# Kernel tuning notes

Measured on AMD Instinct MI355X. Metric: run time of the kernel, lower is better.

The kernel has to match this reference:

```python
import jax, jax.numpy as jnp
import numpy as np

N = 50000          # num nodes
E = 800000         # num edges (avg degree 16)
F_IN = 512         # num_feature
HID = 128          # hid
COM_LAMBDA = 1.0


def setup_inputs() -> dict:
    key = jax.random.key(0)
    k1, k2, k3, k4, k5, k6 = jax.random.split(key, 6)
    v_ori_vals = jax.random.uniform(k1, (E,), dtype=jnp.float32)
    feat = jax.random.normal(k2, (N, F_IN), dtype=jnp.float32)
    v_indices = jax.random.randint(k3, (2, E), 0, N, dtype=jnp.int64)
    # GraphConvolution params
    gcn_w = jax.random.normal(k4, (F_IN, HID), dtype=jnp.float32) / np.sqrt(F_IN)
    gcn_b = jnp.zeros((HID,), dtype=jnp.float32)
    # gen_mlp: Linear(2*hid, 1), xavier_normal init
    std = 1.414 * np.sqrt(2.0 / (2 * HID + 1))
    mlp_w = jax.random.normal(k5, (1, 2 * HID), dtype=jnp.float32) * std
    mlp_b = jnp.zeros((1,), dtype=jnp.float32)
    return {"v_ori_vals": v_ori_vals, "feat": feat, "v_indices": v_indices,
            "num_node": N, "gcn_w": gcn_w, "gcn_b": gcn_b,
            "mlp_w": mlp_w, "mlp_b": mlp_b}


def reference(v_ori_vals, feat, v_indices, num_node, gcn_w, gcn_b, mlp_w, mlp_b):
    row, col = v_indices[0], v_indices[1]
    # gen_gcn: emb = A @ (feat @ W) + b  (SpMM via segment_sum over edges)
    support = feat @ gcn_w                                      # [N, HID]
    emb = jax.ops.segment_sum(v_ori_vals[:, None] * support[col], row,
                              num_segments=num_node) + gcn_b    # [N, HID]
    # gather endpoints, concat, edge-scoring MLP (dropout = identity in eval)
    ff = jnp.concatenate([emb[row], emb[col]], axis=-1)         # [E, 2*HID]
    temp = (ff @ mlp_w.T + mlp_b).reshape(-1)                   # [E]
    # sparse row-wise softmax over columns (dim=1) -> segment softmax by row
    m = jax.ops.segment_max(temp, row, num_segments=num_node)   # [N]
    e = jnp.exp(temp - m[row])                                  # [E]
    s = jax.ops.segment_sum(e, row, num_segments=num_node)      # [N]
    pi = e / s[row]                                             # [E]
    # gen_v = v_ori + com_lambda * pi (values on the shared edge pattern)
    return v_ori_vals + COM_LAMBDA * pi
```

## Files before the change

kernel.cpp:

```cpp
#include <hip/hip_runtime.h>


typedef unsigned int u32;

#define RPB     128
#define CAP     3072
#define NB_MAX  512
#define SB      256

__global__ void k_prep(const float* __restrict__ W, const float* __restrict__ mw,
                       float* __restrict__ u2, u32* __restrict__ cnt,
                       int F, int H, int nb) {
  if (blockIdx.x == 0)
    for (int s = threadIdx.x; s < nb; s += blockDim.x) cnt[s] = 0;
  int f = blockIdx.x * blockDim.x + threadIdx.x;
  if (f >= F) return;
  const float4* wr = (const float4*)(W + (size_t)f * H);
  const float4* mv = (const float4*)(mw + H);
  float s = 0.f;
  for (int i = 0; i < H / 4; ++i) {
    float4 a = wr[i], b = mv[i];
    s = fmaf(a.x, b.x, fmaf(a.y, b.y, fmaf(a.z, b.z, fmaf(a.w, b.w, s))));
  }
  u2[f] = s;
}

template <int F>
__global__ void k_gemv(const float* __restrict__ feat, const float* __restrict__ u2,
                       float* __restrict__ q, int N) {
  const int lane = threadIdx.x & 63;
  const float4 ua = *(const float4*)(u2 + lane * 8);
  const float4 ub = *(const float4*)(u2 + lane * 8 + 4);
  const int wid = (blockIdx.x * blockDim.x + threadIdx.x) >> 6;
  const int nw  = (gridDim.x * blockDim.x) >> 6;
  for (int r = wid; r < N; r += nw) {
    const float* fr = feat + (size_t)r * F + lane * 8;
    float4 a = *(const float4*)fr;
    float4 b = *(const float4*)(fr + 4);
    float s = fmaf(a.x, ua.x, fmaf(a.y, ua.y, fmaf(a.z, ua.z,
              fmaf(a.w, ua.w, fmaf(b.x, ub.x, fmaf(b.y, ub.y,
              fmaf(b.z, ub.z, b.w * ub.w)))))));
    s += __shfl_xor(s, 32);
    s += __shfl_xor(s, 16);
    s += __shfl_xor(s, 8);
    s += __shfl_xor(s, 4);
    s += __shfl_xor(s, 2);
    s += __shfl_xor(s, 1);
    if (lane == 0) q[r] = s;
  }
}

__global__ void __launch_bounds__(1024)
k_sortscatter(const int* __restrict__ row, const int* __restrict__ col,
              const float* __restrict__ v, int E, int chunk,
              u32* __restrict__ cnt, uint2* __restrict__ rec8, int nb) {
  __shared__ u32 h[NB_MAX];
  __shared__ u32 start[NB_MAX];
  const int tid = threadIdx.x;
  for (int s = tid; s < nb; s += blockDim.x) h[s] = 0;
  __syncthreads();
  const int lo = blockIdx.x * chunk;
  const int hi = min(E, lo + chunk);
  for (int e = lo + tid; e < hi; e += blockDim.x)
    atomicAdd(&h[row[e] >> 7], 1u);
  __syncthreads();
  for (int s = tid; s < nb; s += blockDim.x) {
    u32 c = h[s];
    start[s] = c ? atomicAdd(&cnt[s], c) : 0u;
    h[s] = 0u;
  }
  __syncthreads();
  for (int e = lo + tid; e < hi; e += blockDim.x) {
    int r = row[e];
    int b = r >> 7;
    u32 rank = atomicAdd(&h[b], 1u);
    u32 off  = min(start[b] + rank, (u32)CAP - 1);
    rec8[(size_t)b * CAP + off] =
        make_uint2(((u32)col[e] << 7) | (u32)(r & 127),
                   __float_as_uint(v[e]));
  }
}

__global__ void __launch_bounds__(1024)
k_sum_t(const uint2* __restrict__ rec8, const u32* __restrict__ cnt,
        const float* __restrict__ q, float* __restrict__ t) {
  __shared__ float acc[RPB];
  const int b = blockIdx.x;
  const int tid = threadIdx.x;
  if (tid < RPB) acc[tid] = 0.f;
  __syncthreads();
  const u32 lo = (u32)b * CAP;
  const u32 n  = min(cnt[b], (u32)CAP);
  for (u32 i = tid; i < n; i += blockDim.x) {
    uint2 rr = rec8[lo + i];
    atomicAdd(&acc[rr.x & 127], q[rr.x >> 7] * __uint_as_float(rr.y));
  }
  __syncthreads();
  if (tid < RPB) t[b * RPB + tid] = __expf(acc[tid]);
}

__global__ void __launch_bounds__(1024)
k_sum_invS(const uint2* __restrict__ rec8, const u32* __restrict__ cnt,
           const float* __restrict__ t, float* __restrict__ invS) {
  __shared__ float acc[RPB];
  const int b = blockIdx.x;
  const int tid = threadIdx.x;
  if (tid < RPB) acc[tid] = 0.f;
  __syncthreads();
  const u32 lo = (u32)b * CAP;
  const u32 n  = min(cnt[b], (u32)CAP);
  for (u32 i = tid; i < n; i += blockDim.x) {
    uint2 rr = rec8[lo + i];
    atomicAdd(&acc[rr.x & 127], t[rr.x >> 7]);
  }
  __syncthreads();
  if (tid < RPB) invS[b * RPB + tid] = 1.0f / acc[tid];
}

__global__ void k_out(const int* __restrict__ row, const int* __restrict__ col,
                      const float* __restrict__ vori, const float* __restrict__ t,
                      const float* __restrict__ invS, float* __restrict__ out,
                      int E) {
  int e = blockIdx.x * blockDim.x + threadIdx.x;
  if (e >= E) return;
  out[e] = vori[e] + t[col[e]] * invS[row[e]];
}

__global__ void k_scatter_B_at(const int* __restrict__ row, const int* __restrict__ col,
                               const float* __restrict__ v, const float* __restrict__ q,
                               float* __restrict__ B, int E) {
  int e = blockIdx.x * blockDim.x + threadIdx.x;
  if (e >= E) return;
  atomicAdd(&B[row[e]], v[e] * q[col[e]]);
}
__global__ void k_node_t(const float* __restrict__ B, float* __restrict__ t, int N) {
  int n = blockIdx.x * blockDim.x + threadIdx.x;
  if (n < N) t[n] = __expf(B[n]);
}
__global__ void k_scatter_S_at(const int* __restrict__ row, const int* __restrict__ col,
                               const float* __restrict__ t, float* __restrict__ S, int E) {
  int e = blockIdx.x * blockDim.x + threadIdx.x;
  if (e >= E) return;
  atomicAdd(&S[row[e]], t[col[e]]);
}
__global__ void k_out_div(const int* __restrict__ row, const int* __restrict__ col,
                          const float* __restrict__ vori, const float* __restrict__ t,
                          const float* __restrict__ S, float* __restrict__ out, int E) {
  int e = blockIdx.x * blockDim.x + threadIdx.x;
  if (e >= E) return;
  out[e] = vori[e] + t[col[e]] / S[row[e]];
}

extern "C" void kernel_launch(void* const* d_in, const int* in_sizes, int n_in,
                              void* d_out, int out_size, void* d_ws, size_t ws_size,
                              hipStream_t stream) {
  const float* vori = (const float*)d_in[0];
  const float* feat = (const float*)d_in[1];
  const int*   vind = (const int*)d_in[2];
  const float* W    = (const float*)d_in[4];
  const float* mw   = (const float*)d_in[6];

  const int E = in_sizes[0];
  const int H = in_sizes[6] / 2;
  const int F = in_sizes[4] / H;
  const int N = in_sizes[1] / F;

  const int* row = vind;
  const int* col = vind + E;

  const int nb   = (N + RPB - 1) / RPB;
  const int npad = nb * RPB;

  float* ws   = (float*)d_ws;
  float* u2   = ws;
  float* q    = u2 + F;
  float* t    = q + N;
  float* invS = t + npad;
  u32*   cnt  = (u32*)(invS + npad);
  size_t hdr  = (size_t)((char*)(cnt + nb) - (char*)d_ws);
  hdr = (hdr + 15) & ~(size_t)15;
  uint2* rec8 = (uint2*)((char*)d_ws + hdr);
  size_t need = hdr + (size_t)nb * CAP * sizeof(uint2);

  const int eb = (E + 255) / 256;

  k_prep<<<(F + 255) / 256, 256, 0, stream>>>(W, mw, u2, cnt, F, H, nb);
  k_gemv<512><<<3125, 256, 0, stream>>>(feat, u2, q, N);

  if (ws_size >= need && F == 512 && H % 4 == 0 && nb <= NB_MAX) {
    const int chunk = (E + SB - 1) / SB;
    k_sortscatter<<<SB, 1024, 0, stream>>>(row, col, vori, E, chunk, cnt, rec8, nb);
    k_sum_t<<<nb, 1024, 0, stream>>>(rec8, cnt, q, t);
    k_sum_invS<<<nb, 1024, 0, stream>>>(rec8, cnt, t, invS);
    k_out<<<eb, 256, 0, stream>>>(row, col, vori, t, invS, (float*)d_out, E);
  } else {
    const int nbk = (N + 255) / 256;
    float* S = invS;
    hipMemsetAsync((void*)S, 0, sizeof(float) * (size_t)npad, stream);
    k_scatter_B_at<<<eb, 256, 0, stream>>>(row, col, vori, q, S, E);
    k_node_t<<<nbk, 256, 0, stream>>>(S, t, N);
    hipMemsetAsync((void*)S, 0, sizeof(float) * (size_t)npad, stream);
    k_scatter_S_at<<<eb, 256, 0, stream>>>(row, col, t, S, E);
    k_out_div<<<eb, 256, 0, stream>>>(row, col, vori, t, S, (float*)d_out, E);
  }
}
```

Baseline: 217.1 us.

## Fuse GEMV with edge bucket scatter into one launch; vectorize output kernel

Result: faster. 208.4 us (-4.0%).

```diff
diff --git a/kernel.cpp b/kernel.cpp
--- a/kernel.cpp
+++ b/kernel.cpp
@@ -7,6 +7,7 @@
 #define CAP     3072
 #define NB_MAX  512
 #define SB      256
+#define GB      782
 
 __global__ void k_prep(const float* __restrict__ W, const float* __restrict__ mw,
                        float* __restrict__ u2, u32* __restrict__ cnt,
@@ -26,58 +27,61 @@
 }
 
 template <int F>
-__global__ void k_gemv(const float* __restrict__ feat, const float* __restrict__ u2,
-                       float* __restrict__ q, int N) {
-  const int lane = threadIdx.x & 63;
-  const float4 ua = *(const float4*)(u2 + lane * 8);
-  const float4 ub = *(const float4*)(u2 + lane * 8 + 4);
-  const int wid = (blockIdx.x * blockDim.x + threadIdx.x) >> 6;
-  const int nw  = (gridDim.x * blockDim.x) >> 6;
-  for (int r = wid; r < N; r += nw) {
-    const float* fr = feat + (size_t)r * F + lane * 8;
-    float4 a = *(const float4*)fr;
-    float4 b = *(const float4*)(fr + 4);
-    float s = fmaf(a.x, ua.x, fmaf(a.y, ua.y, fmaf(a.z, ua.z,
-              fmaf(a.w, ua.w, fmaf(b.x, ub.x, fmaf(b.y, ub.y,
-              fmaf(b.z, ub.z, b.w * ub.w)))))));
-    s += __shfl_xor(s, 32);
-    s += __shfl_xor(s, 16);
-    s += __shfl_xor(s, 8);
-    s += __shfl_xor(s, 4);
-    s += __shfl_xor(s, 2);
-    s += __shfl_xor(s, 1);
-    if (lane == 0) q[r] = s;
-  }
-}
-
 __global__ void __launch_bounds__(1024)
-k_sortscatter(const int* __restrict__ row, const int* __restrict__ col,
-              const float* __restrict__ v, int E, int chunk,
-              u32* __restrict__ cnt, uint2* __restrict__ rec8, int nb) {
+k_fused(const int* __restrict__ row, const int* __restrict__ col,
+        const float* __restrict__ v, const float* __restrict__ feat,
+        const float* __restrict__ u2, float* __restrict__ q,
+        u32* __restrict__ cnt, uint2* __restrict__ rec8,
+        int E, int N, int nb) {
   __shared__ u32 h[NB_MAX];
   __shared__ u32 start[NB_MAX];
   const int tid = threadIdx.x;
-  for (int s = tid; s < nb; s += blockDim.x) h[s] = 0;
-  __syncthreads();
-  const int lo = blockIdx.x * chunk;
-  const int hi = min(E, lo + chunk);
-  for (int e = lo + tid; e < hi; e += blockDim.x)
-    atomicAdd(&h[row[e] >> 7], 1u);
-  __syncthreads();
-  for (int s = tid; s < nb; s += blockDim.x) {
-    u32 c = h[s];
-    start[s] = c ? atomicAdd(&cnt[s], c) : 0u;
-    h[s] = 0u;
-  }
-  __syncthreads();
-  for (int e = lo + tid; e < hi; e += blockDim.x) {
-    int r = row[e];
-    int b = r >> 7;
-    u32 rank = atomicAdd(&h[b], 1u);
-    u32 off  = min(start[b] + rank, (u32)CAP - 1);
-    rec8[(size_t)b * CAP + off] =
-        make_uint2(((u32)col[e] << 7) | (u32)(r & 127),
-                   __float_as_uint(v[e]));
+
+  if (blockIdx.x < SB) {
+    const int chunk = (E + SB - 1) / SB;
+    for (int s = tid; s < nb; s += blockDim.x) h[s] = 0;
+    __syncthreads();
+    const int lo = blockIdx.x * chunk;
+    const int hi = min(E, lo + chunk);
+    for (int e = lo + tid; e < hi; e += blockDim.x)
+      atomicAdd(&h[row[e] >> 7], 1u);
+    __syncthreads();
+    for (int s = tid; s < nb; s += blockDim.x) {
+      u32 c = h[s];
+      start[s] = c ? atomicAdd(&cnt[s], c) : 0u;
+      h[s] = 0u;
+    }
+    __syncthreads();
+    for (int e = lo + tid; e < hi; e += blockDim.x) {
+      int r = row[e];
+      int b = r >> 7;
+      u32 rank = atomicAdd(&h[b], 1u);
+      u32 off  = min(start[b] + rank, (u32)CAP - 1);
+      rec8[(size_t)b * CAP + off] =
+          make_uint2(((u32)col[e] << 7) | (u32)(r & 127),
+                     __float_as_uint(v[e]));
+    }
+  } else {
+    const int lane = tid & 63;
+    const float4 ua = *(const float4*)(u2 + lane * 8);
+    const float4 ub = *(const float4*)(u2 + lane * 8 + 4);
+    const int wid = (blockIdx.x - SB) * (1024 >> 6) + (tid >> 6);
+    const int nw  = GB * (1024 >> 6);
+    for (int r = wid; r < N; r += nw) {
+      const float* fr = feat + (size_t)r * F + lane * 8;
+      float4 a = *(const float4*)fr;
+      float4 b = *(const float4*)(fr + 4);
+      float s = fmaf(a.x, ua.x, fmaf(a.y, ua.y, fmaf(a.z, ua.z,
+                fmaf(a.w, ua.w, fmaf(b.x, ub.x, fmaf(b.y, ub.y,
+                fmaf(b.z, ub.z, b.w * ub.w)))))));
+      s += __shfl_xor(s, 32);
+      s += __shfl_xor(s, 16);
+      s += __shfl_xor(s, 8);
+      s += __shfl_xor(s, 4);
+      s += __shfl_xor(s, 2);
+      s += __shfl_xor(s, 1);
+      if (lane == 0) q[r] = s;
+    }
   }
 }
 
@@ -121,11 +125,35 @@
                       const float* __restrict__ vori, const float* __restrict__ t,
                       const float* __restrict__ invS, float* __restrict__ out,
                       int E) {
-  int e = blockIdx.x * blockDim.x + threadIdx.x;
-  if (e >= E) return;
-  out[e] = vori[e] + t[col[e]] * invS[row[e]];
-}
-
+  int e4 = blockIdx.x * blockDim.x + threadIdx.x;
+  int e  = e4 * 4;
+  if (e + 3 < E) {
+    int4   r4 = *(const int4*)(row + e);
+    int4   c4 = *(const int4*)(col + e);
+    float4 v4 = *(const float4*)(vori + e);
+    float4 o;
+    o.x = v4.x + t[c4.x] * invS[r4.x];
+    o.y = v4.y + t[c4.y] * invS[r4.y];
+    o.z = v4.z + t[c4.z] * invS[r4.z];
+    o.w = v4.w + t[c4.w] * invS[r4.w];
+    *(float4*)(out + e) = o;
+  } else {
+    for (; e < E; ++e)
+      out[e] = vori[e] + t[col[e]] * invS[row[e]];
+  }
+}
+
+__global__ void k_gemv_fb(const float* __restrict__ feat, const float* __restrict__ u2,
+                          float* __restrict__ q, int N, int F) {
+  const int lane = threadIdx.x & 63;
+  const int wave = (blockIdx.x * blockDim.x + threadIdx.x) >> 6;
+  if (wave >= N) return;
+  const float* fr = feat + (size_t)wave * F;
+  float a = 0.f;
+  for (int i = lane; i < F; i += 64) a = fmaf(fr[i], u2[i], a);
+  for (int off = 32; off; off >>= 1) a += __shfl_xor(a, off);
+  if (lane == 0) q[wave] = a;
+}
 __global__ void k_scatter_B_at(const int* __restrict__ row, const int* __restrict__ col,
                                const float* __restrict__ v, const float* __restrict__ q,
                                float* __restrict__ B, int E) {
@@ -182,20 +210,21 @@
   uint2* rec8 = (uint2*)((char*)d_ws + hdr);
   size_t need = hdr + (size_t)nb * CAP * sizeof(uint2);
 
-  const int eb = (E + 255) / 256;
-
   k_prep<<<(F + 255) / 256, 256, 0, stream>>>(W, mw, u2, cnt, F, H, nb);
-  k_gemv<512><<<3125, 256, 0, stream>>>(feat, u2, q, N);
 
   if (ws_size >= need && F == 512 && H % 4 == 0 && nb <= NB_MAX) {
-    const int chunk = (E + SB - 1) / SB;
-    k_sortscatter<<<SB, 1024, 0, stream>>>(row, col, vori, E, chunk, cnt, rec8, nb);
+    k_fused<512><<<SB + GB, 1024, 0, stream>>>(row, col, vori, feat, u2, q,
+                                               cnt, rec8, E, N, nb);
     k_sum_t<<<nb, 1024, 0, stream>>>(rec8, cnt, q, t);
     k_sum_invS<<<nb, 1024, 0, stream>>>(rec8, cnt, t, invS);
-    k_out<<<eb, 256, 0, stream>>>(row, col, vori, t, invS, (float*)d_out, E);
+    const int e4 = (E + 3) / 4;
+    k_out<<<(e4 + 255) / 256, 256, 0, stream>>>(row, col, vori, t, invS,
+                                                (float*)d_out, E);
   } else {
+    const int eb  = (E + 255) / 256;
     const int nbk = (N + 255) / 256;
     float* S = invS;
+    k_gemv_fb<<<(N * 64 + 255) / 256, 256, 0, stream>>>(feat, u2, q, N, F);
     hipMemsetAsync((void*)S, 0, sizeof(float) * (size_t)npad, stream);
     k_scatter_B_at<<<eb, 256, 0, stream>>>(row, col, vori, q, S, E);
     k_node_t<<<nbk, 256, 0, stream>>>(S, t, N);
```
